# Kernel tuning notes

Measured on AMD Instinct MI355X. Metric: run time of the kernel, lower is better.

## Reference

```python
import jax, jax.numpy as jnp
import numpy as np

HIDDEN = 1024
NUM_HEADS = 16
HEAD_DIM = HIDDEN // NUM_HEADS
SCALING = HEAD_DIM ** -0.5
INF = jnp.finfo(jnp.float32).max


def setup_inputs() -> dict:
    key = jax.random.key(0)
    ks = jax.random.split(key, 16)
    t, b, prev_len = 1, 32, 4095
    inp = {
        "query_input": jax.random.normal(ks[0], (t, b, HIDDEN), jnp.float32),
        "key_input": jax.random.normal(ks[1], (t, b, HIDDEN), jnp.float32),
        "value_input": jax.random.normal(ks[2], (t, b, HIDDEN), jnp.float32),
        "attn_mask": jnp.zeros((t, prev_len + t), jnp.int32),
        "new_state_order": jax.random.randint(ks[3], (b,), 0, b, jnp.int32),
        "prev_key": jax.random.normal(ks[4], (b, NUM_HEADS, prev_len, HEAD_DIM), jnp.float32),
        "prev_value": jax.random.normal(ks[5], (b, NUM_HEADS, prev_len, HEAD_DIM), jnp.float32),
        "Wq": jax.random.normal(ks[6], (HIDDEN, HIDDEN), jnp.float32) * (1.0 / np.sqrt(HIDDEN)),
        "bq": jnp.zeros((HIDDEN,), jnp.float32),
        "Wk": jax.random.normal(ks[7], (HIDDEN, HIDDEN), jnp.float32) * (1.0 / np.sqrt(HIDDEN)),
        "bk": jnp.zeros((HIDDEN,), jnp.float32),
        "Wv": jax.random.normal(ks[8], (HIDDEN, HIDDEN), jnp.float32) * (1.0 / np.sqrt(HIDDEN)),
        "bv": jnp.zeros((HIDDEN,), jnp.float32),
        "Wo": jax.random.normal(ks[9], (HIDDEN, HIDDEN), jnp.float32) * (1.0 / np.sqrt(HIDDEN)),
        "bo": jnp.zeros((HIDDEN,), jnp.float32),
    }
    return inp


def reference(query_input, key_input, value_input, attn_mask, new_state_order,
              prev_key, prev_value, Wq, bq, Wk, bk, Wv, bv, Wo, bo):
    t, b, _ = query_input.shape
    # projections: tf.matmul(x, W, transpose_b=True) -> x @ W.T
    q = (query_input @ Wq.T + bq) * SCALING          # (t, b, H)
    k = key_input @ Wk.T + bk                         # (t, b, H)
    v = value_input @ Wv.T + bv
    # (t, b*nh, hd) -> (b*nh, t, hd)
    q = q.reshape(t, b * NUM_HEADS, HEAD_DIM).transpose(1, 0, 2)
    k = k.reshape(t, b * NUM_HEADS, HEAD_DIM).transpose(1, 0, 2)
    v = v.reshape(t, b * NUM_HEADS, HEAD_DIM).transpose(1, 0, 2)
    # beam reorder of cache, then flatten heads and concat new step
    pk = prev_key[new_state_order].reshape(b * NUM_HEADS, -1, HEAD_DIM)
    pv = prev_value[new_state_order].reshape(b * NUM_HEADS, -1, HEAD_DIM)
    k = jnp.concatenate([pk, k], axis=1)              # (b*nh, S, hd)
    v = jnp.concatenate([pv, v], axis=1)
    # attention scores with additive -INF masking
    scores = jnp.einsum('ntd,nsd->nts', q, k)         # (b*nh, t, S)
    scores = scores - INF * attn_mask.astype(scores.dtype)  # broadcast (t,S)
    w = jax.nn.softmax(scores, axis=2)
    attn = jnp.einsum('nts,nsd->ntd', w, v)           # (b*nh, t, hd)
    attn = attn.transpose(1, 0, 2).reshape(t, b, HIDDEN)
    out = attn @ Wo.T + bo                            # (t, b, H)
    return out
```

## Files before the change

kernel.cpp:

```cpp
#include <hip/hip_runtime.h>

#define HIDDEN  1024
#define NHEADS  16
#define HDIM    64
#define BATCH   32
#define PREV    4095
#define S_TOTAL 4096
#define NSPLIT  8
#define SCHUNK  (S_TOTAL / NSPLIT)
#define SCALING 0.125f
#define FMAX    3.402823466e38f

#define Q_OFF    0
#define K_OFF    32768
#define V_OFF    65536
#define ATTN_OFF 98304
#define PM_OFF   131072
#define PL_OFF   135168
#define PACC_OFF 139264

__global__ __launch_bounds__(256) void init_bias(
    const float* __restrict__ bq, const float* __restrict__ bk,
    const float* __restrict__ bv, const float* __restrict__ bo,
    float* __restrict__ q, float* __restrict__ k, float* __restrict__ v,
    float* __restrict__ out) {
  int i = blockIdx.x * 256 + threadIdx.x;
  int o = i & (HIDDEN - 1);
  q[i] = bq[o]; k[i] = bk[o]; v[i] = bv[o]; out[i] = bo[o];
}

__device__ __forceinline__ void proj_body(const float* __restrict__ x,
                                          const float* __restrict__ W,
                                          float* __restrict__ out) {
  int t  = threadIdx.x;
  int o  = blockIdx.x * 64 + (t & 63);
  int bg = __builtin_amdgcn_readfirstlane(t >> 6);
  int kr = HIDDEN / gridDim.z;
  int k0 = blockIdx.z * kr;
  const float4* wr = (const float4*)(W + (size_t)o * HIDDEN + k0);
  float acc[8];
#pragma unroll
  for (int j = 0; j < 8; ++j) acc[j] = 0.f;
  int n4 = kr >> 2;
  for (int i = 0; i < n4; ++i) {
    float4 w4 = wr[i];
#pragma unroll
    for (int j = 0; j < 8; ++j) {
      const float4* xr = (const float4*)(x + (size_t)(bg * 8 + j) * HIDDEN + k0);
      float4 x4 = xr[i];
      acc[j] = fmaf(w4.x, x4.x, acc[j]);
      acc[j] = fmaf(w4.y, x4.y, acc[j]);
      acc[j] = fmaf(w4.z, x4.z, acc[j]);
      acc[j] = fmaf(w4.w, x4.w, acc[j]);
    }
  }
#pragma unroll
  for (int j = 0; j < 8; ++j)
    unsafeAtomicAdd(&out[(size_t)(bg * 8 + j) * HIDDEN + o], acc[j]);
}

__global__ __launch_bounds__(256) void proj_qkv(
    const float* __restrict__ xq, const float* __restrict__ Wq, float* outq,
    const float* __restrict__ xk, const float* __restrict__ Wk, float* outk,
    const float* __restrict__ xv, const float* __restrict__ Wv, float* outv) {
  const float* x; const float* W; float* out;
  if (blockIdx.y == 0)      { x = xq; W = Wq; out = outq; }
  else if (blockIdx.y == 1) { x = xk; W = Wk; out = outk; }
  else                      { x = xv; W = Wv; out = outv; }
  proj_body(x, W, out);
}

__global__ __launch_bounds__(256) void proj_one(
    const float* __restrict__ x, const float* __restrict__ W, float* out) {
  proj_body(x, W, out);
}

__global__ __launch_bounds__(256) void attn_decode(
    const float* __restrict__ prev_key, const float* __restrict__ prev_value,
    const float* __restrict__ q_ws, const float* __restrict__ k_ws,
    const float* __restrict__ v_ws, const int* __restrict__ order,
    const int* __restrict__ mask, float* __restrict__ part_m,
    float* __restrict__ part_l, float* __restrict__ part_acc) {
  int split = blockIdx.x;
  int head  = blockIdx.y;
  int b = head >> 4, h = head & 15;
  int t = threadIdx.x;
  int bo = order[b];
  int s0 = split * SCHUNK;

  __shared__ float q_sh[HDIM];
  __shared__ float sc[SCHUNK];
  __shared__ float red_m[4];
  __shared__ float red_l[4];
  __shared__ float vred[4][HDIM];

  if (t < HDIM) q_sh[t] = q_ws[(size_t)b * HIDDEN + h * HDIM + t];
  __syncthreads();

  const float4* q4 = (const float4*)q_sh;
  for (int r = t; r < SCHUNK; r += 256) {
    int s = s0 + r;
    const float4* krow = (s < PREV)
        ? (const float4*)(prev_key + ((size_t)(bo * NHEADS + h) * PREV + s) * HDIM)
        : (const float4*)(k_ws + (size_t)b * HIDDEN + h * HDIM);
    float dot = 0.f;
#pragma unroll
    for (int j = 0; j < 16; ++j) {
      float4 kv = krow[j];
      float4 qv = q4[j];
      dot = fmaf(kv.x, qv.x, dot);
      dot = fmaf(kv.y, qv.y, dot);
      dot = fmaf(kv.z, qv.z, dot);
      dot = fmaf(kv.w, qv.w, dot);
    }
    sc[r] = dot * SCALING - FMAX * (float)mask[s];
  }
  __syncthreads();

  float m = -FMAX;
  for (int r = t; r < SCHUNK; r += 256) m = fmaxf(m, sc[r]);
#pragma unroll
  for (int off = 32; off >= 1; off >>= 1) m = fmaxf(m, __shfl_xor(m, off));
  int wid = t >> 6, lane = t & 63;
  if (lane == 0) red_m[wid] = m;
  __syncthreads();
  m = fmaxf(fmaxf(red_m[0], red_m[1]), fmaxf(red_m[2], red_m[3]));

  float lp = 0.f;
  for (int r = t; r < SCHUNK; r += 256) {
    float e = __expf(sc[r] - m);
    sc[r] = e;
    lp += e;
  }
#pragma unroll
  for (int off = 32; off >= 1; off >>= 1) lp += __shfl_xor(lp, off);
  if (lane == 0) red_l[wid] = lp;
  __syncthreads();
  float lb = (red_l[0] + red_l[1]) + (red_l[2] + red_l[3]);

  float acc = 0.f;
  const float* vbase = prev_value + (size_t)(bo * NHEADS + h) * PREV * HDIM;
  int r0 = wid * 128;
#pragma unroll 4
  for (int r = r0; r < r0 + 128; ++r) {
    int s = s0 + r;
    const float* vrow = (s < PREV) ? (vbase + (size_t)s * HDIM)
                                   : (v_ws + (size_t)b * HIDDEN + h * HDIM);
    acc = fmaf(sc[r], vrow[lane], acc);
  }
  vred[wid][lane] = acc;
  __syncthreads();
  if (t < HDIM) {
    float tot = (vred[0][t] + vred[1][t]) + (vred[2][t] + vred[3][t]);
    part_acc[((size_t)head * NSPLIT + split) * HDIM + t] = tot;
  }
  if (t == 0) {
    part_m[head * NSPLIT + split] = m;
    part_l[head * NSPLIT + split] = lb;
  }
}

__global__ __launch_bounds__(64) void attn_combine(
    const float* __restrict__ part_m, const float* __restrict__ part_l,
    const float* __restrict__ part_acc, float* __restrict__ attn) {
  int head = blockIdx.x;
  int d = threadIdx.x;
  float m = -FMAX;
#pragma unroll
  for (int i = 0; i < NSPLIT; ++i) m = fmaxf(m, part_m[head * NSPLIT + i]);
  float L = 0.f, o = 0.f;
#pragma unroll
  for (int i = 0; i < NSPLIT; ++i) {
    float w = __expf(part_m[head * NSPLIT + i] - m);
    L = fmaf(w, part_l[head * NSPLIT + i], L);
    o = fmaf(w, part_acc[((size_t)head * NSPLIT + i) * HDIM + d], o);
  }
  int b = head >> 4, h = head & 15;
  attn[(size_t)b * HIDDEN + h * HDIM + d] = o / L;
}

extern "C" void kernel_launch(void* const* d_in, const int* in_sizes, int n_in,
                              void* d_out, int out_size, void* d_ws, size_t ws_size,
                              hipStream_t stream) {
  const float* qx    = (const float*)d_in[0];
  const float* kx    = (const float*)d_in[1];
  const float* vx    = (const float*)d_in[2];
  const int*   mask  = (const int*)d_in[3];
  const int*   order = (const int*)d_in[4];
  const float* pk    = (const float*)d_in[5];
  const float* pv    = (const float*)d_in[6];
  const float* Wq    = (const float*)d_in[7];
  const float* bq    = (const float*)d_in[8];
  const float* Wk    = (const float*)d_in[9];
  const float* bk    = (const float*)d_in[10];
  const float* Wv    = (const float*)d_in[11];
  const float* bv    = (const float*)d_in[12];
  const float* Wo    = (const float*)d_in[13];
  const float* bo    = (const float*)d_in[14];
  float* out = (float*)d_out;
  float* ws  = (float*)d_ws;

  float* q_ws    = ws + Q_OFF;
  float* k_ws    = ws + K_OFF;
  float* v_ws    = ws + V_OFF;
  float* attn_ws = ws + ATTN_OFF;
  float* pm      = ws + PM_OFF;
  float* pl      = ws + PL_OFF;
  float* pacc    = ws + PACC_OFF;

  hipLaunchKernelGGL(init_bias, dim3(128), dim3(256), 0, stream,
                     bq, bk, bv, bo, q_ws, k_ws, v_ws, out);
  hipLaunchKernelGGL(proj_qkv, dim3(16, 3, 8), dim3(256), 0, stream,
                     qx, Wq, q_ws, kx, Wk, k_ws, vx, Wv, v_ws);
  hipLaunchKernelGGL(attn_decode, dim3(NSPLIT, 512), dim3(256), 0, stream,
                     pk, pv, q_ws, k_ws, v_ws, order, mask, pm, pl, pacc);
  hipLaunchKernelGGL(attn_combine, dim3(512), dim3(64), 0, stream,
                     pm, pl, pacc, attn_ws);
  hipLaunchKernelGGL(proj_one, dim3(16, 1, 16), dim3(256), 0, stream,
                     attn_ws, Wo, out);
}
```

Measured before the change: 1.073 ms.

## Transpose weights for coalesced GEMV and vectorize attention KV loads

Adds a per-call kernel that transposes all four weight matrices into workspace. The projections are rewritten as GEMVs that keep the batch in shared memory and read transposed weight rows with coalesced loads. The attention decode kernel now has 16 lanes share each K/V row through float4 loads and shuffle reductions, and it preloads the mask and pre-scales q. The transpose reads and writes an extra 16 MB per call, and the GEMV grids are smaller, which may leave many compute units idle.

```diff
diff --git a/kernel.cpp b/kernel.cpp
--- a/kernel.cpp
+++ b/kernel.cpp
@@ -11,13 +11,14 @@
 #define SCALING 0.125f
 #define FMAX    3.402823466e38f
 
-#define Q_OFF    0
-#define K_OFF    32768
-#define V_OFF    65536
-#define ATTN_OFF 98304
-#define PM_OFF   131072
-#define PL_OFF   135168
-#define PACC_OFF 139264
+#define WT_OFF   0
+#define Q_OFF    4194304
+#define K_OFF    4227072
+#define V_OFF    4259840
+#define ATTN_OFF 4292608
+#define PM_OFF   4325376
+#define PL_OFF   4329472
+#define PACC_OFF 4333568
 
 __global__ __launch_bounds__(256) void init_bias(
     const float* __restrict__ bq, const float* __restrict__ bk,
@@ -29,50 +30,84 @@
   q[i] = bq[o]; k[i] = bk[o]; v[i] = bv[o]; out[i] = bo[o];
 }
 
-__device__ __forceinline__ void proj_body(const float* __restrict__ x,
-                                          const float* __restrict__ W,
-                                          float* __restrict__ out) {
-  int t  = threadIdx.x;
-  int o  = blockIdx.x * 64 + (t & 63);
-  int bg = __builtin_amdgcn_readfirstlane(t >> 6);
-  int kr = HIDDEN / gridDim.z;
-  int k0 = blockIdx.z * kr;
-  const float4* wr = (const float4*)(W + (size_t)o * HIDDEN + k0);
-  float acc[8];
-#pragma unroll
-  for (int j = 0; j < 8; ++j) acc[j] = 0.f;
-  int n4 = kr >> 2;
-  for (int i = 0; i < n4; ++i) {
-    float4 w4 = wr[i];
-#pragma unroll
-    for (int j = 0; j < 8; ++j) {
-      const float4* xr = (const float4*)(x + (size_t)(bg * 8 + j) * HIDDEN + k0);
-      float4 x4 = xr[i];
-      acc[j] = fmaf(w4.x, x4.x, acc[j]);
-      acc[j] = fmaf(w4.y, x4.y, acc[j]);
-      acc[j] = fmaf(w4.z, x4.z, acc[j]);
-      acc[j] = fmaf(w4.w, x4.w, acc[j]);
+__global__ __launch_bounds__(256) void transpose_w(
+    const float* __restrict__ Wq, const float* __restrict__ Wk,
+    const float* __restrict__ Wv, const float* __restrict__ Wo,
+    float* __restrict__ wt_base) {
+  __shared__ float tile[64][65];
+  int m = blockIdx.y;
+  const float* W = (m == 0) ? Wq : (m == 1) ? Wk : (m == 2) ? Wv : Wo;
+  float* WT = wt_base + (size_t)m * HIDDEN * HIDDEN;
+  int ti = blockIdx.x >> 4, tj = blockIdx.x & 15;
+  int o0 = ti * 64, k0 = tj * 64;
+  int tx = threadIdx.x & 63, ty0 = threadIdx.x >> 6;
+#pragma unroll
+  for (int r = 0; r < 16; ++r) {
+    int row = ty0 + r * 4;
+    tile[row][tx] = W[(size_t)(o0 + row) * HIDDEN + k0 + tx];
+  }
+  __syncthreads();
+#pragma unroll
+  for (int r = 0; r < 16; ++r) {
+    int row = ty0 + r * 4;
+    WT[(size_t)(k0 + row) * HIDDEN + o0 + tx] = tile[tx][row];
+  }
+}
+
+__device__ __forceinline__ void gemv_body(const float* __restrict__ x,
+                                          const float* __restrict__ WT,
+                                          float* __restrict__ out,
+                                          int o0, int k0) {
+  __shared__ __align__(16) float xs[BATCH][64];
+  int t = threadIdx.x;
+#pragma unroll
+  for (int idx = t; idx < BATCH * 64; idx += 256) {
+    int b = idx >> 6, kk = idx & 63;
+    xs[b][kk] = x[(size_t)b * HIDDEN + k0 + kk];
+  }
+  __syncthreads();
+  float acc[BATCH];
+#pragma unroll
+  for (int b = 0; b < BATCH; ++b) acc[b] = 0.f;
+  for (int kk4 = 0; kk4 < 16; ++kk4) {
+    int kk = kk4 * 4;
+    float w0 = WT[(size_t)(k0 + kk + 0) * HIDDEN + o0 + t];
+    float w1 = WT[(size_t)(k0 + kk + 1) * HIDDEN + o0 + t];
+    float w2 = WT[(size_t)(k0 + kk + 2) * HIDDEN + o0 + t];
+    float w3 = WT[(size_t)(k0 + kk + 3) * HIDDEN + o0 + t];
+#pragma unroll
+    for (int b = 0; b < BATCH; ++b) {
+      float4 xv = *(const float4*)&xs[b][kk];
+      float a = acc[b];
+      a = fmaf(xv.x, w0, a);
+      a = fmaf(xv.y, w1, a);
+      a = fmaf(xv.z, w2, a);
+      a = fmaf(xv.w, w3, a);
+      acc[b] = a;
     }
   }
 #pragma unroll
-  for (int j = 0; j < 8; ++j)
-    unsafeAtomicAdd(&out[(size_t)(bg * 8 + j) * HIDDEN + o], acc[j]);
-}
-
-__global__ __launch_bounds__(256) void proj_qkv(
-    const float* __restrict__ xq, const float* __restrict__ Wq, float* outq,
-    const float* __restrict__ xk, const float* __restrict__ Wk, float* outk,
-    const float* __restrict__ xv, const float* __restrict__ Wv, float* outv) {
-  const float* x; const float* W; float* out;
-  if (blockIdx.y == 0)      { x = xq; W = Wq; out = outq; }
-  else if (blockIdx.y == 1) { x = xk; W = Wk; out = outk; }
-  else                      { x = xv; W = Wv; out = outv; }
-  proj_body(x, W, out);
-}
-
-__global__ __launch_bounds__(256) void proj_one(
-    const float* __restrict__ x, const float* __restrict__ W, float* out) {
-  proj_body(x, W, out);
+  for (int b = 0; b < BATCH; ++b)
+    unsafeAtomicAdd(&out[(size_t)b * HIDDEN + o0 + t], acc[b]);
+}
+
+__global__ __launch_bounds__(256) void gemv_qkv(
+    const float* __restrict__ xq, const float* __restrict__ xk,
+    const float* __restrict__ xv, const float* __restrict__ wt_base,
+    float* __restrict__ outq, float* __restrict__ outk,
+    float* __restrict__ outv) {
+  const float* x; const float* WT; float* out;
+  if (blockIdx.y == 0)      { x = xq; WT = wt_base;                        out = outq; }
+  else if (blockIdx.y == 1) { x = xk; WT = wt_base + 1 * HIDDEN * HIDDEN;  out = outk; }
+  else                      { x = xv; WT = wt_base + 2 * HIDDEN * HIDDEN;  out = outv; }
+  gemv_body(x, WT, out, blockIdx.x * 256, blockIdx.z * 64);
+}
+
+__global__ __launch_bounds__(256) void gemv_o(
+    const float* __restrict__ x, const float* __restrict__ wt_base,
+    float* __restrict__ out) {
+  gemv_body(x, wt_base + (size_t)3 * HIDDEN * HIDDEN, out,
+            blockIdx.x * 256, blockIdx.z * 64);
 }
 
 __global__ __launch_bounds__(256) void attn_decode(
@@ -85,70 +120,84 @@
   int head  = blockIdx.y;
   int b = head >> 4, h = head & 15;
   int t = threadIdx.x;
+  int w = t >> 6, lane = t & 63;
+  int rg = lane >> 4, qg = lane & 15;
   int bo = order[b];
   int s0 = split * SCHUNK;
 
-  __shared__ float q_sh[HDIM];
   __shared__ float sc[SCHUNK];
+  __shared__ float msk[SCHUNK];
   __shared__ float red_m[4];
   __shared__ float red_l[4];
-  __shared__ float vred[4][HDIM];
-
-  if (t < HDIM) q_sh[t] = q_ws[(size_t)b * HIDDEN + h * HDIM + t];
-  __syncthreads();
-
-  const float4* q4 = (const float4*)q_sh;
-  for (int r = t; r < SCHUNK; r += 256) {
+  __shared__ __align__(16) float vred[4][HDIM];
+
+  msk[t]       = -FMAX * (float)mask[s0 + t];
+  msk[t + 256] = -FMAX * (float)mask[s0 + t + 256];
+
+  float4 qs = *(const float4*)(q_ws + (size_t)b * HIDDEN + h * HDIM + (qg << 2));
+  qs.x *= SCALING; qs.y *= SCALING; qs.z *= SCALING; qs.w *= SCALING;
+
+  size_t kvbase = (size_t)(bo * NHEADS + h) * PREV * HDIM;
+  const float* kws_row = k_ws + (size_t)b * HIDDEN + h * HDIM;
+  const float* vws_row = v_ws + (size_t)b * HIDDEN + h * HDIM;
+  __syncthreads();
+
+  for (int it = 0; it < 32; ++it) {
+    int r = w * 128 + it * 4 + rg;
     int s = s0 + r;
-    const float4* krow = (s < PREV)
-        ? (const float4*)(prev_key + ((size_t)(bo * NHEADS + h) * PREV + s) * HDIM)
-        : (const float4*)(k_ws + (size_t)b * HIDDEN + h * HDIM);
-    float dot = 0.f;
-#pragma unroll
-    for (int j = 0; j < 16; ++j) {
-      float4 kv = krow[j];
-      float4 qv = q4[j];
-      dot = fmaf(kv.x, qv.x, dot);
-      dot = fmaf(kv.y, qv.y, dot);
-      dot = fmaf(kv.z, qv.z, dot);
-      dot = fmaf(kv.w, qv.w, dot);
-    }
-    sc[r] = dot * SCALING - FMAX * (float)mask[s];
-  }
-  __syncthreads();
-
-  float m = -FMAX;
-  for (int r = t; r < SCHUNK; r += 256) m = fmaxf(m, sc[r]);
+    const float* kp = (s < PREV) ? (prev_key + kvbase + (size_t)s * HDIM)
+                                 : kws_row;
+    float4 kv = *(const float4*)(kp + (qg << 2));
+    float d = kv.x * qs.x;
+    d = fmaf(kv.y, qs.y, d);
+    d = fmaf(kv.z, qs.z, d);
+    d = fmaf(kv.w, qs.w, d);
+    d += __shfl_xor(d, 1);
+    d += __shfl_xor(d, 2);
+    d += __shfl_xor(d, 4);
+    d += __shfl_xor(d, 8);
+    if (qg == 0) sc[r] = d + msk[r];
+  }
+  __syncthreads();
+
+  float m = fmaxf(sc[t], sc[t + 256]);
 #pragma unroll
   for (int off = 32; off >= 1; off >>= 1) m = fmaxf(m, __shfl_xor(m, off));
-  int wid = t >> 6, lane = t & 63;
-  if (lane == 0) red_m[wid] = m;
+  if (lane == 0) red_m[w] = m;
   __syncthreads();
   m = fmaxf(fmaxf(red_m[0], red_m[1]), fmaxf(red_m[2], red_m[3]));
 
-  float lp = 0.f;
-  for (int r = t; r < SCHUNK; r += 256) {
-    float e = __expf(sc[r] - m);
-    sc[r] = e;
-    lp += e;
-  }
+  float e0 = __expf(sc[t] - m);
+  float e1 = __expf(sc[t + 256] - m);
+  sc[t] = e0; sc[t + 256] = e1;
+  float lp = e0 + e1;
 #pragma unroll
   for (int off = 32; off >= 1; off >>= 1) lp += __shfl_xor(lp, off);
-  if (lane == 0) red_l[wid] = lp;
+  if (lane == 0) red_l[w] = lp;
   __syncthreads();
   float lb = (red_l[0] + red_l[1]) + (red_l[2] + red_l[3]);
 
-  float acc = 0.f;
-  const float* vbase = prev_value + (size_t)(bo * NHEADS + h) * PREV * HDIM;
-  int r0 = wid * 128;
-#pragma unroll 4
-  for (int r = r0; r < r0 + 128; ++r) {
+  float4 av = {0.f, 0.f, 0.f, 0.f};
+  for (int it = 0; it < 32; ++it) {
+    int r = w * 128 + it * 4 + rg;
     int s = s0 + r;
-    const float* vrow = (s < PREV) ? (vbase + (size_t)s * HDIM)
-                                   : (v_ws + (size_t)b * HIDDEN + h * HDIM);
-    acc = fmaf(sc[r], vrow[lane], acc);
-  }
-  vred[wid][lane] = acc;
+    const float* vp = (s < PREV) ? (prev_value + kvbase + (size_t)s * HDIM)
+                                 : vws_row;
+    float4 vv = *(const float4*)(vp + (qg << 2));
+    float wgt = sc[r];
+    av.x = fmaf(wgt, vv.x, av.x);
+    av.y = fmaf(wgt, vv.y, av.y);
+    av.z = fmaf(wgt, vv.z, av.z);
+    av.w = fmaf(wgt, vv.w, av.w);
+  }
+#pragma unroll
+  for (int off = 16; off <= 32; off <<= 1) {
+    av.x += __shfl_xor(av.x, off);
+    av.y += __shfl_xor(av.y, off);
+    av.z += __shfl_xor(av.z, off);
+    av.w += __shfl_xor(av.w, off);
+  }
+  if (rg == 0) *(float4*)&vred[w][qg << 2] = av;
   __syncthreads();
   if (t < HDIM) {
     float tot = (vred[0][t] + vred[1][t]) + (vred[2][t] + vred[3][t]);
@@ -200,6 +249,7 @@
   float* out = (float*)d_out;
   float* ws  = (float*)d_ws;
 
+  float* wt      = ws + WT_OFF;
   float* q_ws    = ws + Q_OFF;
   float* k_ws    = ws + K_OFF;
   float* v_ws    = ws + V_OFF;
@@ -210,12 +260,14 @@
 
   hipLaunchKernelGGL(init_bias, dim3(128), dim3(256), 0, stream,
                      bq, bk, bv, bo, q_ws, k_ws, v_ws, out);
-  hipLaunchKernelGGL(proj_qkv, dim3(16, 3, 8), dim3(256), 0, stream,
-                     qx, Wq, q_ws, kx, Wk, k_ws, vx, Wv, v_ws);
+  hipLaunchKernelGGL(transpose_w, dim3(256, 4), dim3(256), 0, stream,
+                     Wq, Wk, Wv, Wo, wt);
+  hipLaunchKernelGGL(gemv_qkv, dim3(4, 3, 16), dim3(256), 0, stream,
+                     qx, kx, vx, wt, q_ws, k_ws, v_ws);
   hipLaunchKernelGGL(attn_decode, dim3(NSPLIT, 512), dim3(256), 0, stream,
                      pk, pv, q_ws, k_ws, v_ws, order, mask, pm, pl, pacc);
   hipLaunchKernelGGL(attn_combine, dim3(512), dim3(64), 0, stream,
                      pm, pl, pacc, attn_ws);
-  hipLaunchKernelGGL(proj_one, dim3(16, 1, 16), dim3(256), 0, stream,
-                     attn_ws, Wo, out);
-}
+  hipLaunchKernelGGL(gemv_o, dim3(4, 1, 16), dim3(256), 0, stream,
+                     attn_ws, wt, out);
+}
```

Result: faster. 1.035 ms (-3.6%).
